# Optimization experiments

Hardware: AMD Instinct MI355X
Metric: run time of the kernel (lower is better)

## Reference

```python
import jax, jax.numpy as jnp
import numpy as np

B, T, C, NH = 4, 2048, 1024, 16
HD = C // NH  # head dim = 64


def setup_inputs() -> dict:
    key = jax.random.key(0)
    ks = jax.random.split(key, 5)
    s = 0.02
    return {
        "x": jax.random.normal(ks[0], (B, T, C), dtype=jnp.float32),
        "W_attn": jax.random.normal(ks[1], (C, 3 * C), dtype=jnp.float32) * s,
        "b_attn": jnp.zeros((3 * C,), dtype=jnp.float32),
        "W_proj": jax.random.normal(ks[2], (C, C), dtype=jnp.float32) * s,
        "b_proj": jnp.zeros((C,), dtype=jnp.float32),
    }


def reference(x, W_attn, b_attn, W_proj, b_proj):
    Bv, Tv, Cv = x.shape
    qkv = x @ W_attn + b_attn  # [B,T,3C]
    q, k, v = jnp.split(qkv, 3, axis=2)
    # [B,T,C] -> [B,NH,T,HD]
    def heads(t):
        return t.reshape(Bv, Tv, NH, HD).transpose(0, 2, 1, 3)
    q, k, v = heads(q), heads(k), heads(v)
    scores = jnp.einsum("bhqd,bhkd->bhqk", q, k) / jnp.sqrt(jnp.float32(HD))
    causal = jnp.tril(jnp.ones((Tv, Tv), dtype=bool))
    scores = jnp.where(causal[None, None, :, :], scores, jnp.float32(-jnp.inf))
    probs = jax.nn.softmax(scores, axis=-1)
    # dropout rate is 0.0 -> identity
    y = jnp.einsum("bhqk,bhkd->bhqd", probs, v)
    y = y.transpose(0, 2, 1, 3).reshape(Bv, Tv, Cv)
    return y @ W_proj + b_proj
```

## Files before the change

kernel.cpp:

```cpp
#include <hip/hip_runtime.h>
#include <hip/hip_bf16.h>

#define Bsz 4
#define Tseq 2048
#define Cdim 1024
#define NH 16
#define HD 64
#define Mrows (Bsz*Tseq)
#define N3C (3*Cdim)

typedef __attribute__((ext_vector_type(8))) short short8;
typedef __attribute__((ext_vector_type(4))) short short4v;
typedef __attribute__((ext_vector_type(4))) float float4v;

__device__ __forceinline__ unsigned short f2b(float f) {
    union { float f; unsigned u; } x; x.f = f;
    unsigned u = x.u;
    u += 0x7fff + ((u >> 16) & 1);
    return (unsigned short)(u >> 16);
}

__device__ __forceinline__ float lo_b(unsigned u) {
    union { unsigned x; float f; } c; c.x = u << 16; return c.f;
}
__device__ __forceinline__ float hi_b(unsigned u) {
    union { unsigned x; float f; } c; c.x = u & 0xffff0000u; return c.f;
}

__device__ __forceinline__ unsigned pk2bf(float a, float b) {
#if __has_builtin(__builtin_amdgcn_cvt_pk_bf16_f32)
    auto w = __builtin_amdgcn_cvt_pk_bf16_f32(a, b);
    unsigned u; __builtin_memcpy(&u, &w, 4);
    return u;
#else
    return (unsigned)f2b(a) | ((unsigned)f2b(b) << 16);
#endif
}

#define GLDS(gp, lp) __builtin_amdgcn_global_load_lds(                         \
    (const __attribute__((address_space(1))) unsigned*)(gp),                   \
    (__attribute__((address_space(3))) unsigned*)(lp), 16, 0, 0)

__global__ __launch_bounds__(256) void cast_kernel(const float* __restrict__ in,
                                                   unsigned short* __restrict__ out, int n) {
    int i = (blockIdx.x * 256 + threadIdx.x) * 4;
    if (i < n) {
        float4 v = *reinterpret_cast<const float4*>(in + i);
        ushort4 o;
        o.x = f2b(v.x); o.y = f2b(v.y); o.z = f2b(v.z); o.w = f2b(v.w);
        *reinterpret_cast<ushort4*>(out + i) = o;
    }
}

__global__ __launch_bounds__(256) void transpose_cast(const float* __restrict__ in,
                                                      unsigned short* __restrict__ out,
                                                      int K, int N) {
    __shared__ float tile[32][33];
    int n0 = blockIdx.x * 32, k0 = blockIdx.y * 32;
    int tx = threadIdx.x & 31, ty = threadIdx.x >> 5;
    #pragma unroll
    for (int i = 0; i < 32; i += 8)
        tile[ty + i][tx] = in[(k0 + ty + i) * N + n0 + tx];
    __syncthreads();
    #pragma unroll
    for (int i = 0; i < 32; i += 8)
        out[(size_t)(n0 + ty + i) * K + k0 + tx] = f2b(tile[tx][ty + i]);
}


template<bool QKV, int NCOL>
__global__ __launch_bounds__(256) void gemm_bt(const unsigned short* __restrict__ A,
                                               const unsigned short* __restrict__ Bt,
                                               const float* __restrict__ bias,
                                               unsigned short* __restrict__ qb,
                                               unsigned short* __restrict__ kb,
                                               unsigned short* __restrict__ vb,
                                               float* __restrict__ out) {
    __shared__ unsigned short As[128 * 32];
    __shared__ unsigned short Bs[128 * 32];
    int tid = threadIdx.x;
    int lane = tid & 63, wave = tid >> 6;
    int wm = wave >> 1, wn = wave & 1;
    int l15 = lane & 15, quad = lane >> 4;

    int f = blockIdx.x;
    int xcd = f & 7, slot = f >> 3;
    int rowblk = xcd * 8 + (slot & 7);
    int colblk = slot >> 3;
    int row0 = rowblk * 128;
    int col0 = colblk * 128;

    int sr = tid >> 2, sk = (tid & 3) * 8;
    const unsigned short* Ag = A + (size_t)(row0 + sr) * Cdim + sk;
    const unsigned short* Bg = Bt + (size_t)(col0 + sr) * Cdim + sk;
    unsigned short* Al = &As[wave * 512];
    unsigned short* Bl = &Bs[wave * 512];

    float4v acc[4][4] = {};

    for (int k0 = 0; k0 < Cdim; k0 += 32) {
        __syncthreads();
        GLDS(Ag + k0,             Al);
        GLDS(Ag + k0 + 64 * Cdim, Al + 2048);
        GLDS(Bg + k0,             Bl);
        GLDS(Bg + k0 + 64 * Cdim, Bl + 2048);
        __syncthreads();

        short8 af[4], bf[4];
        #pragma unroll
        for (int mi = 0; mi < 4; mi++)
            af[mi] = *(const short8*)&As[(wm * 64 + mi * 16 + l15) * 32 + quad * 8];
        #pragma unroll
        for (int ni = 0; ni < 4; ni++)
            bf[ni] = *(const short8*)&Bs[(wn * 64 + ni * 16 + l15) * 32 + quad * 8];
        #pragma unroll
        for (int mi = 0; mi < 4; mi++)
            #pragma unroll
            for (int ni = 0; ni < 4; ni++)
                acc[mi][ni] = __builtin_amdgcn_mfma_f32_16x16x32_bf16(af[mi], bf[ni], acc[mi][ni], 0, 0, 0);
    }

    #pragma unroll
    for (int mi = 0; mi < 4; mi++) {
        #pragma unroll
        for (int ni = 0; ni < 4; ni++) {
            int colb = col0 + wn * 64 + ni * 16 + l15;
            int rowb = row0 + wm * 64 + mi * 16 + quad * 4;
            if (QKV) {
                int p = colb >> 10;
                int h = (colb & 1023) >> 6;
                int d = colb & 63;
                int b = rowb >> 11;
                int t = rowb & 2047;
                if (p == 2) {
                    ushort4 pk;
                    pk.x = f2b(acc[mi][ni][0] + bias[colb]);
                    pk.y = f2b(acc[mi][ni][1] + bias[colb]);
                    pk.z = f2b(acc[mi][ni][2] + bias[colb]);
                    pk.w = f2b(acc[mi][ni][3] + bias[colb]);
                    *(ushort4*)&vb[((size_t)(b * NH + h) * HD + d) * Tseq + t] = pk;
                } else {
                    unsigned short* dst = (p == 0) ? qb : kb;
                    #pragma unroll
                    for (int r = 0; r < 4; r++)
                        dst[((size_t)(b * NH + h) * Tseq + (t + r)) * HD + d] =
                            f2b(acc[mi][ni][r] + bias[colb]);
                }
            } else {
                #pragma unroll
                for (int r = 0; r < 4; r++)
                    out[(size_t)(rowb + r) * Cdim + colb] = acc[mi][ni][r] + bias[colb];
            }
        }
    }
}

#define LDK 72

__global__ __launch_bounds__(128, 4) void attn_kernel(const unsigned short* __restrict__ qb,
                                                      const unsigned short* __restrict__ kb,
                                                      const unsigned short* __restrict__ vt,
                                                      unsigned short* __restrict__ yb) {
    __shared__ unsigned short Ks[64 * LDK];
    __shared__ unsigned short Vs[64 * LDK];

    int tid = threadIdx.x;
    int lane = tid & 63, wave = tid >> 6;
    int l15 = lane & 15, quad = lane >> 4;
    int bh = blockIdx.x;
    int qt = 31 - blockIdx.y;

    const unsigned short* Qh = qb + (size_t)bh * Tseq * HD;
    const unsigned short* Kh = kb + (size_t)bh * Tseq * HD;
    const unsigned short* Vh = vt + (size_t)bh * HD * Tseq;
    int b = bh >> 4, h = bh & 15;

    int srow = tid >> 1, sc = (tid & 1) * 32;
    const float cexp = 0.18033688011112042f;

    int q0 = qt * 64;
    int rb0 = q0 + wave * 32;

    short8 qf[2][2];
    #pragma unroll
    for (int mi = 0; mi < 2; mi++)
        #pragma unroll
        for (int g = 0; g < 2; g++)
            qf[mi][g] = *(const short8*)(Qh + (size_t)(rb0 + mi * 16 + l15) * HD + g * 32 + quad * 8);

    float4v ov[2][4] = {};
    float m[2]  = {-1e30f, -1e30f};
    float lp[2] = {0.f, 0.f};
    int ntiles = qt + 1;

    for (int jt = 0; jt < ntiles; jt++) {
        int j0 = jt * 64;
        __syncthreads();
        const unsigned short* Kg = Kh + (size_t)(j0 + srow) * HD + sc;
        const unsigned short* Vg = Vh + (size_t)srow * Tseq + j0 + sc;
        #pragma unroll
        for (int u = 0; u < 4; u++) {
            *(short8*)&Ks[srow * LDK + sc + u * 8] = *(const short8*)(Kg + u * 8);
            *(short8*)&Vs[srow * LDK + sc + u * 8] = *(const short8*)(Vg + u * 8);
        }
        __syncthreads();

        float4v st[2][4];
        #pragma unroll
        for (int mi = 0; mi < 2; mi++)
            #pragma unroll
            for (int kg = 0; kg < 4; kg++)
                st[mi][kg] = (float4v){0.f, 0.f, 0.f, 0.f};
        #pragma unroll
        for (int g = 0; g < 2; g++) {
            #pragma unroll
            for (int kg = 0; kg < 4; kg++) {
                short8 kf = *(const short8*)&Ks[(kg * 16 + l15) * LDK + g * 32 + quad * 8];
                st[0][kg] = __builtin_amdgcn_mfma_f32_16x16x32_bf16(kf, qf[0][g], st[0][kg], 0, 0, 0);
                st[1][kg] = __builtin_amdgcn_mfma_f32_16x16x32_bf16(kf, qf[1][g], st[1][kg], 0, 0, 0);
            }
        }

        if (jt == ntiles - 1) {
            #pragma unroll
            for (int mi = 0; mi < 2; mi++) {
                int qrow = rb0 + mi * 16 + l15;
                #pragma unroll
                for (int kg = 0; kg < 4; kg++) {
                    int keyb = j0 + kg * 16 + quad * 4;
                    #pragma unroll
                    for (int r = 0; r < 4; r++)
                        if (keyb + r > qrow) st[mi][kg][r] = -1e30f;
                }
            }
        }

        short4v pf[2][4];
        #pragma unroll
        for (int mi = 0; mi < 2; mi++) {
            float mx = st[mi][0][0];
            #pragma unroll
            for (int kg = 0; kg < 4; kg++)
                #pragma unroll
                for (int r = 0; r < 4; r++)
                    mx = fmaxf(mx, st[mi][kg][r]);
            mx = fmaxf(mx, __shfl_xor(mx, 16));
            mx = fmaxf(mx, __shfl_xor(mx, 32));
            float mn = fmaxf(m[mi], mx);
            if (__any(mn > m[mi])) {
                float alv = __builtin_amdgcn_exp2f((m[mi] - mn) * cexp);
                m[mi] = mn;
                lp[mi] *= alv;
                float ar_[4];
                #pragma unroll
                for (int r = 0; r < 4; r++)
                    ar_[r] = __shfl(alv, quad * 4 + r);
                #pragma unroll
                for (int dg = 0; dg < 4; dg++)
                    #pragma unroll
                    for (int r = 0; r < 4; r++)
                        ov[mi][dg][r] *= ar_[r];
            }
            float sum = 0.f;
            #pragma unroll
            for (int kg = 0; kg < 4; kg++) {
                float p0 = __builtin_amdgcn_exp2f((st[mi][kg][0] - m[mi]) * cexp);
                float p1 = __builtin_amdgcn_exp2f((st[mi][kg][1] - m[mi]) * cexp);
                float p2 = __builtin_amdgcn_exp2f((st[mi][kg][2] - m[mi]) * cexp);
                float p3 = __builtin_amdgcn_exp2f((st[mi][kg][3] - m[mi]) * cexp);
                unsigned u0 = pk2bf(p0, p1);
                unsigned u1 = pk2bf(p2, p3);
                sum += (lo_b(u0) + hi_b(u0)) + (lo_b(u1) + hi_b(u1));
                union { unsigned u[2]; short4v s; } pk_;
                pk_.u[0] = u0; pk_.u[1] = u1;
                pf[mi][kg] = pk_.s;
            }
            lp[mi] += sum;
        }

        #pragma unroll
        for (int kg = 0; kg < 4; kg++) {
            #pragma unroll
            for (int dg = 0; dg < 4; dg++) {
                short4v vf = *(const short4v*)&Vs[(dg * 16 + l15) * LDK + kg * 16 + quad * 4];
                ov[0][dg] = __builtin_amdgcn_mfma_f32_16x16x16bf16_1k(pf[0][kg], vf, ov[0][dg], 0, 0, 0);
                ov[1][dg] = __builtin_amdgcn_mfma_f32_16x16x16bf16_1k(pf[1][kg], vf, ov[1][dg], 0, 0, 0);
            }
        }
    }

    #pragma unroll
    for (int mi = 0; mi < 2; mi++) {
        float lf = lp[mi];
        lf += __shfl_xor(lf, 16);
        lf += __shfl_xor(lf, 32);
        float rinv[4];
        #pragma unroll
        for (int r = 0; r < 4; r++)
            rinv[r] = 1.0f / __shfl(lf, quad * 4 + r);
        #pragma unroll
        for (int dg = 0; dg < 4; dg++)
            #pragma unroll
            for (int r = 0; r < 4; r++) {
                int t = rb0 + mi * 16 + quad * 4 + r;
                yb[((size_t)b * Tseq + t) * Cdim + h * HD + dg * 16 + l15] =
                    f2b(ov[mi][dg][r] * rinv[r]);
            }
    }
}

extern "C" void kernel_launch(void* const* d_in, const int* in_sizes, int n_in,
                              void* d_out, int out_size, void* d_ws, size_t ws_size,
                              hipStream_t stream) {
    const float* x  = (const float*)d_in[0];
    const float* Wa = (const float*)d_in[1];
    const float* ba = (const float*)d_in[2];
    const float* Wp = (const float*)d_in[3];
    const float* bp = (const float*)d_in[4];
    float* out = (float*)d_out;

    unsigned short* ws = (unsigned short*)d_ws;
    unsigned short* xb  = ws;
    unsigned short* Wat = xb  + (size_t)Mrows * Cdim;
    unsigned short* Wpt = Wat + (size_t)N3C * Cdim;
    unsigned short* qb  = Wpt + (size_t)Cdim * Cdim;
    unsigned short* kb  = qb  + (size_t)Bsz * NH * Tseq * HD;
    unsigned short* vb  = kb  + (size_t)Bsz * NH * Tseq * HD;
    unsigned short* yb  = vb  + (size_t)Bsz * NH * Tseq * HD;

    int nx = Mrows * Cdim;
    cast_kernel<<<nx / 4 / 256, 256, 0, stream>>>(x, xb, nx);
    transpose_cast<<<dim3(N3C / 32, Cdim / 32), 256, 0, stream>>>(Wa, Wat, Cdim, N3C);
    transpose_cast<<<dim3(Cdim / 32, Cdim / 32), 256, 0, stream>>>(Wp, Wpt, Cdim, Cdim);

    gemm_bt<true, 24><<<64 * 24, 256, 0, stream>>>(
        xb, Wat, ba, qb, kb, vb, nullptr);

    attn_kernel<<<dim3(Bsz * NH, 32), 128, 0, stream>>>(qb, kb, vb, yb);

    gemm_bt<false, 8><<<64 * 8, 256, 0, stream>>>(
        yb, Wpt, bp, nullptr, nullptr, nullptr, out);
}
```

Measured before the change: 291.7 us.

## Widen GEMM K-step with padded LDS; per-wave K staging and direct V loads in attention

The GEMM now stages 64-wide K slices per iteration into padded LDS rows, so it needs half as many barrier pairs and avoids bank conflicts on fragment reads. The attention kernel drops block-wide barriers. Each wave stages its own copy of the K tile via direct global-to-LDS loads, and V fragments are read straight from global memory into registers instead of through shared memory. This adds register pressure (launch bound occupancy lowered from 4 to 3) and redundant K/V global traffic per wave.

```diff
diff --git a/kernel.cpp b/kernel.cpp
--- a/kernel.cpp
+++ b/kernel.cpp
@@ -68,6 +68,8 @@
 }
 
 
+#define GROW(r) ((r) * 64 + ((r) >> 3) * 8)
+
 template<bool QKV, int NCOL>
 __global__ __launch_bounds__(256) void gemm_bt(const unsigned short* __restrict__ A,
                                                const unsigned short* __restrict__ Bt,
@@ -76,8 +78,8 @@
                                                unsigned short* __restrict__ kb,
                                                unsigned short* __restrict__ vb,
                                                float* __restrict__ out) {
-    __shared__ unsigned short As[128 * 32];
-    __shared__ unsigned short Bs[128 * 32];
+    __shared__ unsigned short As[8320];
+    __shared__ unsigned short Bs[8320];
     int tid = threadIdx.x;
     int lane = tid & 63, wave = tid >> 6;
     int wm = wave >> 1, wn = wave & 1;
@@ -90,34 +92,37 @@
     int row0 = rowblk * 128;
     int col0 = colblk * 128;
 
-    int sr = tid >> 2, sk = (tid & 3) * 8;
-    const unsigned short* Ag = A + (size_t)(row0 + sr) * Cdim + sk;
-    const unsigned short* Bg = Bt + (size_t)(col0 + sr) * Cdim + sk;
-    unsigned short* Al = &As[wave * 512];
-    unsigned short* Bl = &Bs[wave * 512];
+    const unsigned short* Ag = A + (size_t)(row0 + wave * 32 + (lane >> 3)) * Cdim + (lane & 7) * 8;
+    const unsigned short* Bg = Bt + (size_t)(col0 + wave * 32 + (lane >> 3)) * Cdim + (lane & 7) * 8;
+    unsigned short* Al = &As[wave * 2080];
+    unsigned short* Bl = &Bs[wave * 2080];
 
     float4v acc[4][4] = {};
 
-    for (int k0 = 0; k0 < Cdim; k0 += 32) {
+    for (int k0 = 0; k0 < Cdim; k0 += 64) {
         __syncthreads();
-        GLDS(Ag + k0,             Al);
-        GLDS(Ag + k0 + 64 * Cdim, Al + 2048);
-        GLDS(Bg + k0,             Bl);
-        GLDS(Bg + k0 + 64 * Cdim, Bl + 2048);
+        #pragma unroll
+        for (int c = 0; c < 4; c++) {
+            GLDS(Ag + k0 + (size_t)(c * 8) * Cdim, Al + c * 520);
+            GLDS(Bg + k0 + (size_t)(c * 8) * Cdim, Bl + c * 520);
+        }
         __syncthreads();
 
-        short8 af[4], bf[4];
-        #pragma unroll
-        for (int mi = 0; mi < 4; mi++)
-            af[mi] = *(const short8*)&As[(wm * 64 + mi * 16 + l15) * 32 + quad * 8];
-        #pragma unroll
-        for (int ni = 0; ni < 4; ni++)
-            bf[ni] = *(const short8*)&Bs[(wn * 64 + ni * 16 + l15) * 32 + quad * 8];
-        #pragma unroll
-        for (int mi = 0; mi < 4; mi++)
+        #pragma unroll
+        for (int g = 0; g < 2; g++) {
+            short8 af[4], bf[4];
+            #pragma unroll
+            for (int mi = 0; mi < 4; mi++)
+                af[mi] = *(const short8*)&As[GROW(wm * 64 + mi * 16 + l15) + g * 32 + quad * 8];
             #pragma unroll
             for (int ni = 0; ni < 4; ni++)
-                acc[mi][ni] = __builtin_amdgcn_mfma_f32_16x16x32_bf16(af[mi], bf[ni], acc[mi][ni], 0, 0, 0);
+                bf[ni] = *(const short8*)&Bs[GROW(wn * 64 + ni * 16 + l15) + g * 32 + quad * 8];
+            #pragma unroll
+            for (int mi = 0; mi < 4; mi++)
+                #pragma unroll
+                for (int ni = 0; ni < 4; ni++)
+                    acc[mi][ni] = __builtin_amdgcn_mfma_f32_16x16x32_bf16(af[mi], bf[ni], acc[mi][ni], 0, 0, 0);
+        }
     }
 
     #pragma unroll
@@ -155,14 +160,12 @@
     }
 }
 
-#define LDK 72
-
-__global__ __launch_bounds__(128, 4) void attn_kernel(const unsigned short* __restrict__ qb,
+
+__global__ __launch_bounds__(128, 3) void attn_kernel(const unsigned short* __restrict__ qb,
                                                       const unsigned short* __restrict__ kb,
                                                       const unsigned short* __restrict__ vt,
                                                       unsigned short* __restrict__ yb) {
-    __shared__ unsigned short Ks[64 * LDK];
-    __shared__ unsigned short Vs[64 * LDK];
+    __shared__ unsigned short Ks[2][64 * 64];
 
     int tid = threadIdx.x;
     int lane = tid & 63, wave = tid >> 6;
@@ -174,8 +177,6 @@
     const unsigned short* Kh = kb + (size_t)bh * Tseq * HD;
     const unsigned short* Vh = vt + (size_t)bh * HD * Tseq;
     int b = bh >> 4, h = bh & 15;
-
-    int srow = tid >> 1, sc = (tid & 1) * 32;
     const float cexp = 0.18033688011112042f;
 
     int q0 = qt * 64;
@@ -187,6 +188,10 @@
         #pragma unroll
         for (int g = 0; g < 2; g++)
             qf[mi][g] = *(const short8*)(Qh + (size_t)(rb0 + mi * 16 + l15) * HD + g * 32 + quad * 8);
+
+    const unsigned short* Kg = Kh + (size_t)(lane >> 3) * HD + (lane & 7) * 8;
+    unsigned short* Kl = &Ks[wave][0];
+    const unsigned short* Vg = Vh + (size_t)l15 * Tseq + quad * 4;
 
     float4v ov[2][4] = {};
     float m[2]  = {-1e30f, -1e30f};
@@ -195,15 +200,19 @@
 
     for (int jt = 0; jt < ntiles; jt++) {
         int j0 = jt * 64;
-        __syncthreads();
-        const unsigned short* Kg = Kh + (size_t)(j0 + srow) * HD + sc;
-        const unsigned short* Vg = Vh + (size_t)srow * Tseq + j0 + sc;
-        #pragma unroll
-        for (int u = 0; u < 4; u++) {
-            *(short8*)&Ks[srow * LDK + sc + u * 8] = *(const short8*)(Kg + u * 8);
-            *(short8*)&Vs[srow * LDK + sc + u * 8] = *(const short8*)(Vg + u * 8);
-        }
-        __syncthreads();
+        asm volatile("s_waitcnt lgkmcnt(0)" ::: "memory");
+        #pragma unroll
+        for (int c = 0; c < 8; c++)
+            GLDS(Kg + (size_t)(j0 + c * 8) * HD, Kl + c * 512);
+
+        short4v vf[4][4];
+        #pragma unroll
+        for (int dg = 0; dg < 4; dg++)
+            #pragma unroll
+            for (int kg = 0; kg < 4; kg++)
+                vf[dg][kg] = *(const short4v*)(Vg + (size_t)(dg * 16) * Tseq + j0 + kg * 16);
+
+        asm volatile("s_waitcnt vmcnt(0)" ::: "memory");
 
         float4v st[2][4];
         #pragma unroll
@@ -215,7 +224,7 @@
         for (int g = 0; g < 2; g++) {
             #pragma unroll
             for (int kg = 0; kg < 4; kg++) {
-                short8 kf = *(const short8*)&Ks[(kg * 16 + l15) * LDK + g * 32 + quad * 8];
+                short8 kf = *(const short8*)&Kl[(kg * 16 + l15) * 64 + g * 32 + quad * 8];
                 st[0][kg] = __builtin_amdgcn_mfma_f32_16x16x32_bf16(kf, qf[0][g], st[0][kg], 0, 0, 0);
                 st[1][kg] = __builtin_amdgcn_mfma_f32_16x16x32_bf16(kf, qf[1][g], st[1][kg], 0, 0, 0);
             }
@@ -282,9 +291,8 @@
         for (int kg = 0; kg < 4; kg++) {
             #pragma unroll
             for (int dg = 0; dg < 4; dg++) {
-                short4v vf = *(const short4v*)&Vs[(dg * 16 + l15) * LDK + kg * 16 + quad * 4];
-                ov[0][dg] = __builtin_amdgcn_mfma_f32_16x16x16bf16_1k(pf[0][kg], vf, ov[0][dg], 0, 0, 0);
-                ov[1][dg] = __builtin_amdgcn_mfma_f32_16x16x16bf16_1k(pf[1][kg], vf, ov[1][dg], 0, 0, 0);
+                ov[0][dg] = __builtin_amdgcn_mfma_f32_16x16x16bf16_1k(pf[0][kg], vf[dg][kg], ov[0][dg], 0, 0, 0);
+                ov[1][dg] = __builtin_amdgcn_mfma_f32_16x16x16bf16_1k(pf[1][kg], vf[dg][kg], ov[1][dg], 0, 0, 0);
             }
         }
     }
```

New measurement: 362.0 us. +24.1%, slower.
